# Performance work log

Measured on AMD Instinct MI355X. Metric: run time of the kernel, lower is better.

Reference implementation:

```python
import jax, jax.numpy as jnp
import numpy as np

BN_EPS = 1e-5


def setup_inputs() -> dict:
    key = jax.random.key(0)
    ks = jax.random.split(key, 9)
    B, C, H, W = 2, 64, 128, 128
    Ci = 32  # inter_channels
    sc = 0.05
    x = jax.random.normal(ks[0], (B, C, H, W), jnp.float32)
    g_w = jax.random.normal(ks[1], (Ci, C), jnp.float32) * sc
    g_b = jax.random.normal(ks[2], (Ci,), jnp.float32) * sc
    theta_w = jax.random.normal(ks[3], (Ci, C), jnp.float32) * sc
    theta_b = jax.random.normal(ks[4], (Ci,), jnp.float32) * sc
    phi_w = jax.random.normal(ks[5], (Ci, C), jnp.float32) * sc
    phi_b = jax.random.normal(ks[6], (Ci,), jnp.float32) * sc
    w_w = jax.random.normal(ks[7], (C, Ci), jnp.float32) * sc
    w_b = jnp.zeros((C,), jnp.float32)
    # BatchNorm affine params (random so the block is non-trivial; the torch
    # code zero-inits them, which would make the whole block an identity).
    bn_gamma = 1.0 + 0.1 * jax.random.normal(ks[8], (C,), jnp.float32)
    bn_beta = jnp.zeros((C,), jnp.float32)
    return dict(x=x, g_w=g_w, g_b=g_b, theta_w=theta_w, theta_b=theta_b,
                phi_w=phi_w, phi_b=phi_b, w_w=w_w, w_b=w_b,
                bn_gamma=bn_gamma, bn_beta=bn_beta)


def reference(x, g_w, g_b, theta_w, theta_b, phi_w, phi_b, w_w, w_b,
              bn_gamma, bn_beta):
    B, C, H, W = x.shape
    Ci = g_w.shape[0]
    H1, W1 = H // 2, W // 2

    def block(xq):  # embedded-gaussian non-local block on one quadrant group [B,C,h,w]
        b, c, h, w = xq.shape
        n = h * w
        xf = xq.reshape(b, c, n)                                  # [B,C,N]
        th = jnp.einsum('oc,bcn->bno', theta_w, xf) + theta_b     # [B,N,Ci]
        ph = jnp.einsum('oc,bcn->bon', phi_w, xf) + phi_b[:, None]  # [B,Ci,N]
        gx = jnp.einsum('oc,bcn->bno', g_w, xf) + g_b             # [B,N,Ci]
        f = jnp.einsum('bno,bom->bnm', th, ph)                    # [B,N,N] affinity
        a = jax.nn.softmax(f, axis=-1)
        y = jnp.einsum('bnm,bmo->bno', a, gx)                     # [B,N,Ci]
        wy = jnp.einsum('co,bno->bcn', w_w, y) + w_b[:, None]     # [B,C,N]
        wy = wy.reshape(b, c, h, w)
        # BatchNorm2d, training-mode batch stats (per quadrant call in torch)
        mu = wy.mean(axis=(0, 2, 3), keepdims=True)
        var = wy.var(axis=(0, 2, 3), keepdims=True)
        bn = (wy - mu) * jax.lax.rsqrt(var + BN_EPS)
        bn = bn * bn_gamma[None, :, None, None] + bn_beta[None, :, None, None]
        return bn + xq                                            # residual

    # split into 4 quadrants: [B,C,H,W] -> [4,B,C,H1,W1] (quadrant-major)
    xq = x.reshape(B, C, 2, H1, 2, W1).transpose(2, 4, 0, 1, 3, 5)
    xq = xq.reshape(4, B, C, H1, W1)
    zq = jax.vmap(block)(xq)                                      # [4,B,C,H1,W1]
    # reassemble
    z = zq.reshape(2, 2, B, C, H1, W1).transpose(2, 3, 0, 4, 1, 5)
    return z.reshape(B, C, H, W)
```

## Files before the change

kernel.cpp:

```cpp
#include <hip/hip_runtime.h>
#include <stdint.h>

typedef __bf16 bf16x8 __attribute__((ext_vector_type(8)));
typedef short  short4v __attribute__((ext_vector_type(4)));
typedef float  floatx4 __attribute__((ext_vector_type(4)));
typedef uint32_t u32x4 __attribute__((ext_vector_type(4)));

#define DI __device__ __forceinline__

DI uint16_t bf1(float a) {
    union { __bf16 h; uint16_t u; } r; r.h = (__bf16)a; return r.u;
}

__global__ __launch_bounds__(256) void proj_kernel(
    const float* __restrict__ x,
    const float* __restrict__ tw, const float* __restrict__ tb,
    const float* __restrict__ pw, const float* __restrict__ pb,
    const float* __restrict__ gw, const float* __restrict__ gb,
    uint16_t* __restrict__ th, uint16_t* __restrict__ phT,
    uint16_t* __restrict__ vP)
{
    __shared__ uint16_t ldsg[32 * 68];
    int nt = blockIdx.x & 63, blk = blockIdx.x >> 6;
    int tid = threadIdx.x, wid = tid >> 6, lane = tid & 63;
    int quad = lane >> 4, low = lane & 15;

    int b = blk & 1, q = blk >> 1, qh = q >> 1, qw = q & 1;
    int pixA = wid * 16 + low;
    const float* xg = x + (size_t)b * 1048576 +
                      (size_t)(qh * 64 + nt) * 128 + qw * 64 + pixA;

    float a0[8], a1[8];
#pragma unroll
    for (int j = 0; j < 8; ++j) {
        a0[j] = xg[(size_t)(quad * 8 + j) * 16384];
        a1[j] = xg[(size_t)(32 + quad * 8 + j) * 16384];
    }
    bf16x8 A0, A1;
#pragma unroll
    for (int j = 0; j < 8; ++j) {
        A0[j] = (__bf16)a0[j];
        A1[j] = (__bf16)a1[j];
    }

    auto dotile = [&](const float* W, const float* Bv, int o0) -> floatx4 {
        floatx4 acc;
        float bias = Bv[o0 + low];
#pragma unroll
        for (int r = 0; r < 4; ++r) acc[r] = bias;
        const float* wr = W + (o0 + low) * 64 + quad * 8;
        floatx4 w0a = *(const floatx4*)(wr);
        floatx4 w0b = *(const floatx4*)(wr + 4);
        floatx4 w1a = *(const floatx4*)(wr + 32);
        floatx4 w1b = *(const floatx4*)(wr + 36);
        bf16x8 B0, B1;
#pragma unroll
        for (int j = 0; j < 4; ++j) {
            B0[j]     = (__bf16)w0a[j];
            B0[j + 4] = (__bf16)w0b[j];
            B1[j]     = (__bf16)w1a[j];
            B1[j + 4] = (__bf16)w1b[j];
        }
        acc = __builtin_amdgcn_mfma_f32_16x16x32_bf16(A0, B0, acc, 0, 0, 0);
        acc = __builtin_amdgcn_mfma_f32_16x16x32_bf16(A1, B1, acc, 0, 0, 0);
        return acc;
    };

    size_t thbase = ((size_t)blk * 4096 + nt * 64 + wid * 16 + quad * 4) * 32;

    floatx4 t0 = dotile(tw, tb, 0), t1 = dotile(tw, tb, 16);
#pragma unroll
    for (int r = 0; r < 4; ++r) {
        th[thbase + r * 32 + low]      = bf1(t0[r] * 1.44269504088896f);
        th[thbase + r * 32 + 16 + low] = bf1(t1[r] * 1.44269504088896f);
    }
    floatx4 p0 = dotile(pw, pb, 0), p1 = dotile(pw, pb, 16);
#pragma unroll
    for (int r = 0; r < 4; ++r) {
        phT[thbase + r * 32 + low]      = bf1(p0[r]);
        phT[thbase + r * 32 + 16 + low] = bf1(p1[r]);
    }
    floatx4 g0 = dotile(gw, gb, 0), g1 = dotile(gw, gb, 16);
#pragma unroll
    for (int r = 0; r < 4; ++r) {
        ldsg[(low)      * 68 + wid * 16 + quad * 4 + r] = bf1(g0[r]);
        ldsg[(16 + low) * 68 + wid * 16 + quad * 4 + r] = bf1(g1[r]);
    }
    __syncthreads();
    {
        int o = tid >> 3, k = (tid & 7) * 8;
        const uint16_t* src = &ldsg[o * 68 + k];
        uint64_t lo = *(const uint64_t*)(src);
        uint64_t hi = *(const uint64_t*)(src + 4);
        union { uint64_t q[2]; u32x4 v; } out;
        out.q[0] = lo; out.q[1] = hi;
        *(u32x4*)(vP + (size_t)blk * 131072 + nt * 2048 + tid * 8) = out.v;
    }
}

__global__ __launch_bounds__(512, 2) void flash_kernel(
    const uint16_t* __restrict__ th, const uint16_t* __restrict__ phT,
    const uint16_t* __restrict__ vP, const float* __restrict__ w_w,
    const float* __restrict__ w_b, float* __restrict__ wy,
    float2* __restrict__ partials)
{
    __shared__ uint16_t ldsK[2][2][2][64 * 40];
    __shared__ uint16_t ldsV[2][2][2][32 * 72];
    __shared__ float sred[4][64][2];
    int blk = blockIdx.x & 7;
    int rg  = blockIdx.x >> 3;
    int tid = threadIdx.x, wid = tid >> 6, lane = tid & 63;
    int half = wid >> 2, w4 = wid & 3;
    int ltid = tid & 255;
    int quad = lane >> 4, low = lane & 15;
    int n0 = rg * 128 + w4 * 32;

    const uint16_t* thB = th  + (size_t)blk * 131072;
    const uint16_t* kG  = phT + (size_t)blk * 131072;
    const uint16_t* vG  = vP  + (size_t)blk * 131072;

    bf16x8 qfA = *(const bf16x8*)(thB + (n0 + low) * 32 + quad * 8);
    bf16x8 qfB = *(const bf16x8*)(thB + (n0 + 16 + low) * 32 + quad * 8);

    const int kWr = (ltid >> 2) * 40 + (ltid & 3) * 8;
    const int vWr = (ltid >> 3) * 72 + (ltid & 7) * 8;
    const u32x4* kSrc = (const u32x4*)kG + half * 8192 + ltid;
    const u32x4* vSrc = (const u32x4*)vG + half * 8192 + ltid;

    u32x4 kr0 = kSrc[0],  kr1 = kSrc[256];
    u32x4 vr0 = vSrc[0],  vr1 = vSrc[256];
    *(u32x4*)(&ldsK[half][0][0][kWr]) = kr0;  *(u32x4*)(&ldsK[half][0][1][kWr]) = kr1;
    *(u32x4*)(&ldsV[half][0][0][vWr]) = vr0;  *(u32x4*)(&ldsV[half][0][1][vWr]) = vr1;
    __syncthreads();

    floatx4 zero = {0.f, 0.f, 0.f, 0.f};
    floatx4 oaA0 = zero, oaA1 = zero, osA = zero;
    floatx4 oaB0 = zero, oaB1 = zero, osB = zero;
    union { uint32_t u[2]; short4v v; } ones;
    ones.u[0] = 0x3F803F80u; ones.u[1] = 0x3F803F80u;

    for (int t = 0; t < 16; ++t) {
        int buf = t & 1;
        if (t < 15) {
            kr0 = kSrc[(2*t + 2) * 256]; kr1 = kSrc[(2*t + 3) * 256];
            vr0 = vSrc[(2*t + 2) * 256]; vr1 = vSrc[(2*t + 3) * 256];
        }
#pragma unroll
        for (int s = 0; s < 2; ++s) {
            const uint16_t* Kb = ldsK[half][buf][s];
            const uint16_t* Vb = ldsV[half][buf][s];
            bf16x8  kf[4]; short4v va[4], vb[4];
#pragma unroll
            for (int c = 0; c < 4; ++c) {
                kf[c] = *(const bf16x8*)(Kb + (c * 16 + low) * 40 + quad * 8);
                va[c] = *(const short4v*)(Vb + low * 72 + c * 16 + quad * 4);
                vb[c] = *(const short4v*)(Vb + (16 + low) * 72 + c * 16 + quad * 4);
            }
            floatx4 saA[4], saB[4];
#pragma unroll
            for (int c = 0; c < 4; ++c) {
                saA[c] = __builtin_amdgcn_mfma_f32_16x16x32_bf16(kf[c], qfA, zero, 0, 0, 0);
                saB[c] = __builtin_amdgcn_mfma_f32_16x16x32_bf16(kf[c], qfB, zero, 0, 0, 0);
            }
            union { __bf16 h[4]; short4v v; } PA[4], PB[4];
#pragma unroll
            for (int c = 0; c < 4; ++c) {
                PA[c].h[0] = (__bf16)__builtin_amdgcn_exp2f(saA[c][0]);
                PA[c].h[1] = (__bf16)__builtin_amdgcn_exp2f(saA[c][1]);
                PA[c].h[2] = (__bf16)__builtin_amdgcn_exp2f(saA[c][2]);
                PA[c].h[3] = (__bf16)__builtin_amdgcn_exp2f(saA[c][3]);
                PB[c].h[0] = (__bf16)__builtin_amdgcn_exp2f(saB[c][0]);
                PB[c].h[1] = (__bf16)__builtin_amdgcn_exp2f(saB[c][1]);
                PB[c].h[2] = (__bf16)__builtin_amdgcn_exp2f(saB[c][2]);
                PB[c].h[3] = (__bf16)__builtin_amdgcn_exp2f(saB[c][3]);
            }
#pragma unroll
            for (int c = 0; c < 4; ++c) {
                oaA0 = __builtin_amdgcn_mfma_f32_16x16x16bf16_1k(va[c], PA[c].v, oaA0, 0, 0, 0);
                oaB0 = __builtin_amdgcn_mfma_f32_16x16x16bf16_1k(va[c], PB[c].v, oaB0, 0, 0, 0);
                oaA1 = __builtin_amdgcn_mfma_f32_16x16x16bf16_1k(vb[c], PA[c].v, oaA1, 0, 0, 0);
                oaB1 = __builtin_amdgcn_mfma_f32_16x16x16bf16_1k(vb[c], PB[c].v, oaB1, 0, 0, 0);
                osA  = __builtin_amdgcn_mfma_f32_16x16x16bf16_1k(ones.v, PA[c].v, osA, 0, 0, 0);
                osB  = __builtin_amdgcn_mfma_f32_16x16x16bf16_1k(ones.v, PB[c].v, osB, 0, 0, 0);
            }
        }
        if (t < 15) {
            *(u32x4*)(&ldsK[half][buf ^ 1][0][kWr]) = kr0;
            *(u32x4*)(&ldsK[half][buf ^ 1][1][kWr]) = kr1;
            *(u32x4*)(&ldsV[half][buf ^ 1][0][vWr]) = vr0;
            *(u32x4*)(&ldsV[half][buf ^ 1][1][vWr]) = vr1;
        }
        __syncthreads();
    }

    {
        float* exM = (float*)(&ldsK[half][0][0][0]);
        int li = ltid * 18;
#pragma unroll
        for (int r = 0; r < 4; ++r) {
            exM[li + r]      = oaA0[r];
            exM[li + 4 + r]  = oaA1[r];
            exM[li + 9 + r]  = oaB0[r];
            exM[li + 13 + r] = oaB1[r];
        }
        exM[li + 8]  = osA[0];
        exM[li + 17] = osB[0];
    }
    __syncthreads();
    const float* exO = (const float*)(&ldsK[half ^ 1][0][0][0]);
    float osA0 = osA[0] + exO[ltid * 18 + 8];
    float osB0 = osB[0] + exO[ltid * 18 + 17];
#pragma unroll
    for (int r = 0; r < 4; ++r) {
        oaA0[r] += exO[ltid * 18 + r];
        oaA1[r] += exO[ltid * 18 + 4 + r];
        oaB0[r] += exO[ltid * 18 + 9 + r];
        oaB1[r] += exO[ltid * 18 + 13 + r];
    }

    float rinvA = 1.0f / osA0, rinvB = 1.0f / osB0;
    union { __bf16 h[4]; short4v v; } YA0, YA1, YB0, YB1;
#pragma unroll
    for (int r = 0; r < 4; ++r) {
        YA0.h[r] = (__bf16)(oaA0[r] * rinvA);
        YA1.h[r] = (__bf16)(oaA1[r] * rinvA);
        YB0.h[r] = (__bf16)(oaB0[r] * rinvB);
        YB1.h[r] = (__bf16)(oaB1[r] * rinvB);
    }

    float* wyB = wy + (size_t)blk * 262144;
    int nA = n0 + low, nB = n0 + 16 + low;
#pragma unroll
    for (int cc = 0; cc < 2; ++cc) {
        int ct = half * 2 + cc;
        floatx4 accA, accB;
#pragma unroll
        for (int r = 0; r < 4; ++r) {
            accA[r] = w_b[ct * 16 + quad * 4 + r];
            accB[r] = accA[r];
        }
        floatx4 w0 = *(const floatx4*)(w_w + (ct * 16 + low) * 32 + quad * 4);
        floatx4 w1 = *(const floatx4*)(w_w + (ct * 16 + low) * 32 + 16 + quad * 4);
        union { __bf16 h[4]; short4v v; } W0, W1;
#pragma unroll
        for (int r = 0; r < 4; ++r) {
            W0.h[r] = (__bf16)w0[r];
            W1.h[r] = (__bf16)w1[r];
        }
        accA = __builtin_amdgcn_mfma_f32_16x16x16bf16_1k(W0.v, YA0.v, accA, 0, 0, 0);
        accA = __builtin_amdgcn_mfma_f32_16x16x16bf16_1k(W1.v, YA1.v, accA, 0, 0, 0);
        accB = __builtin_amdgcn_mfma_f32_16x16x16bf16_1k(W0.v, YB0.v, accB, 0, 0, 0);
        accB = __builtin_amdgcn_mfma_f32_16x16x16bf16_1k(W1.v, YB1.v, accB, 0, 0, 0);
#pragma unroll
        for (int r = 0; r < 4; ++r) {
            int ch = ct * 16 + quad * 4 + r;
            wyB[(size_t)ch * 4096 + nA] = accA[r];
            wyB[(size_t)ch * 4096 + nB] = accB[r];
            float s = accA[r] + accB[r];
            float ss = accA[r] * accA[r] + accB[r] * accB[r];
            s += __shfl_xor(s, 1); ss += __shfl_xor(ss, 1);
            s += __shfl_xor(s, 2); ss += __shfl_xor(ss, 2);
            s += __shfl_xor(s, 4); ss += __shfl_xor(ss, 4);
            s += __shfl_xor(s, 8); ss += __shfl_xor(ss, 8);
            if (low == 0) {
                sred[w4][ch][0] = s;
                sred[w4][ch][1] = ss;
            }
        }
    }
    __syncthreads();
    if (tid < 64) {
        float s  = sred[0][tid][0] + sred[1][tid][0] + sred[2][tid][0] + sred[3][tid][0];
        float ss = sred[0][tid][1] + sred[1][tid][1] + sred[2][tid][1] + sred[3][tid][1];
        partials[((size_t)blk * 32 + rg) * 64 + tid] = make_float2(s, ss);
    }
}

__global__ __launch_bounds__(64) void stats_kernel(
    const float2* __restrict__ partials, const float* __restrict__ gamma,
    const float* __restrict__ beta, float2* __restrict__ stats)
{
    int q = blockIdx.x >> 6, c = blockIdx.x & 63;
    int t = threadIdx.x;
    int b = t >> 5, rg = t & 31;
    int blk = q * 2 + b;
    float2 p = partials[((size_t)blk * 32 + rg) * 64 + c];
    float S = p.x, SS = p.y;
    S += __shfl_xor(S, 1);  SS += __shfl_xor(SS, 1);
    S += __shfl_xor(S, 2);  SS += __shfl_xor(SS, 2);
    S += __shfl_xor(S, 4);  SS += __shfl_xor(SS, 4);
    S += __shfl_xor(S, 8);  SS += __shfl_xor(SS, 8);
    S += __shfl_xor(S, 16); SS += __shfl_xor(SS, 16);
    S += __shfl_xor(S, 32); SS += __shfl_xor(SS, 32);
    if (t == 0) {
        float mu  = S * (1.0f / 8192.0f);
        float var = SS * (1.0f / 8192.0f) - mu * mu;
        float scale = gamma[c] * rsqrtf(var + 1e-5f);
        float shift = beta[c] - mu * scale;
        stats[q * 64 + c] = make_float2(scale, shift);
    }
}

__global__ __launch_bounds__(256) void final_kernel(
    const float* __restrict__ wy, const float2* __restrict__ stats,
    const float* __restrict__ x, float* __restrict__ out)
{
    size_t base = ((size_t)blockIdx.x * 256 + threadIdx.x) * 4;
    int n   = (int)(base & 4095);
    int c   = (int)((base >> 12) & 63);
    int blk = (int)(base >> 18);
    int b = blk & 1, q = blk >> 1, qh = q >> 1, qw = q & 1;
    int i = n >> 6, j = n & 63;
    float2 sc = stats[q * 64 + c];
    floatx4 wv = *(const floatx4*)(wy + base);
    size_t xa = ((size_t)(b * 64 + c) * 128 + (qh * 64 + i)) * 128 + qw * 64 + j;
    floatx4 xv = *(const floatx4*)(x + xa);
    floatx4 ov;
#pragma unroll
    for (int k = 0; k < 4; ++k) ov[k] = wv[k] * sc.x + sc.y + xv[k];
    *(floatx4*)(out + xa) = ov;
}

extern "C" void kernel_launch(void* const* d_in, const int* in_sizes, int n_in,
                              void* d_out, int out_size, void* d_ws, size_t ws_size,
                              hipStream_t stream)
{
    const float* x       = (const float*)d_in[0];
    const float* g_w     = (const float*)d_in[1];
    const float* g_b     = (const float*)d_in[2];
    const float* theta_w = (const float*)d_in[3];
    const float* theta_b = (const float*)d_in[4];
    const float* phi_w   = (const float*)d_in[5];
    const float* phi_b   = (const float*)d_in[6];
    const float* w_w     = (const float*)d_in[7];
    const float* w_b     = (const float*)d_in[8];
    const float* gamma   = (const float*)d_in[9];
    const float* beta    = (const float*)d_in[10];

    char* ws = (char*)d_ws;
    uint16_t* th       = (uint16_t*)(ws);
    uint16_t* phT      = (uint16_t*)(ws + (2u << 20));
    uint16_t* vP       = (uint16_t*)(ws + (4u << 20));
    float*    wy       = (float*)(ws + (6u << 20));
    float2*   partials = (float2*)(ws + (14u << 20));
    float2*   stats    = (float2*)(ws + (14u << 20) + (1u << 18));

    proj_kernel  <<<512,  256, 0, stream>>>(x, theta_w, theta_b, phi_w, phi_b,
                                            g_w, g_b, th, phT, vP);
    flash_kernel <<<256,  512, 0, stream>>>(th, phT, vP, w_w, w_b, wy, partials);
    stats_kernel <<<256,  64,  0, stream>>>(partials, gamma, beta, stats);
    final_kernel <<<2048, 256, 0, stream>>>(wy, stats, x, (float*)d_out);
}
```

Baseline: 128.1 us.

## Split flash kernel keys four ways over half-size query tiles, doubling grid

The flash kernel now handles 64 query rows per block instead of 128 and splits the key sequence into four spans, one per wave pair, instead of two. The grid doubles to 512 blocks and the launch bounds request four blocks per CU, which is meant to raise occupancy and latency hiding across the machine. The cross-span reduction becomes a four-way LDS sum, and each wave pair now computes only one channel tile of the output projection. The stats kernel is updated for the new partials layout. The trade-off is more redundant K/V loading per query row and tighter register limits, which could cause spills.

```diff
diff --git a/kernel.cpp b/kernel.cpp
--- a/kernel.cpp
+++ b/kernel.cpp
@@ -98,22 +98,22 @@
     }
 }
 
-__global__ __launch_bounds__(512, 2) void flash_kernel(
+__global__ __launch_bounds__(512, 4) void flash_kernel(
     const uint16_t* __restrict__ th, const uint16_t* __restrict__ phT,
     const uint16_t* __restrict__ vP, const float* __restrict__ w_w,
     const float* __restrict__ w_b, float* __restrict__ wy,
     float2* __restrict__ partials)
 {
-    __shared__ uint16_t ldsK[2][2][2][64 * 40];
-    __shared__ uint16_t ldsV[2][2][2][32 * 72];
-    __shared__ float sred[4][64][2];
+    __shared__ uint16_t ldsK[4][2][64 * 40];
+    __shared__ uint16_t ldsV[4][2][32 * 72];
+    __shared__ float sred[2][64][2];
     int blk = blockIdx.x & 7;
     int rg  = blockIdx.x >> 3;
     int tid = threadIdx.x, wid = tid >> 6, lane = tid & 63;
-    int half = wid >> 2, w4 = wid & 3;
-    int ltid = tid & 255;
+    int sp = wid >> 1, qg = wid & 1;
+    int lt = tid & 127;
     int quad = lane >> 4, low = lane & 15;
-    int n0 = rg * 128 + w4 * 32;
+    int n0 = rg * 64 + qg * 32;
 
     const uint16_t* thB = th  + (size_t)blk * 131072;
     const uint16_t* kG  = phT + (size_t)blk * 131072;
@@ -122,15 +122,17 @@
     bf16x8 qfA = *(const bf16x8*)(thB + (n0 + low) * 32 + quad * 8);
     bf16x8 qfB = *(const bf16x8*)(thB + (n0 + 16 + low) * 32 + quad * 8);
 
-    const int kWr = (ltid >> 2) * 40 + (ltid & 3) * 8;
-    const int vWr = (ltid >> 3) * 72 + (ltid & 7) * 8;
-    const u32x4* kSrc = (const u32x4*)kG + half * 8192 + ltid;
-    const u32x4* vSrc = (const u32x4*)vG + half * 8192 + ltid;
-
-    u32x4 kr0 = kSrc[0],  kr1 = kSrc[256];
-    u32x4 vr0 = vSrc[0],  vr1 = vSrc[256];
-    *(u32x4*)(&ldsK[half][0][0][kWr]) = kr0;  *(u32x4*)(&ldsK[half][0][1][kWr]) = kr1;
-    *(u32x4*)(&ldsV[half][0][0][vWr]) = vr0;  *(u32x4*)(&ldsV[half][0][1][vWr]) = vr1;
+    const u32x4* kSrc = (const u32x4*)kG + sp * 4096 + lt;
+    const u32x4* vSrc = (const u32x4*)vG + sp * 4096 + lt;
+    const int kW0 = ((lt >> 2)) * 40 + (lt & 3) * 8;
+    const int kW1 = (32 + (lt >> 2)) * 40 + (lt & 3) * 8;
+    const int vW0 = ((lt >> 3)) * 72 + (lt & 7) * 8;
+    const int vW1 = (16 + (lt >> 3)) * 72 + (lt & 7) * 8;
+
+    u32x4 kr0 = kSrc[0], kr1 = kSrc[128];
+    u32x4 vr0 = vSrc[0], vr1 = vSrc[128];
+    *(u32x4*)(&ldsK[sp][0][kW0]) = kr0;  *(u32x4*)(&ldsK[sp][0][kW1]) = kr1;
+    *(u32x4*)(&ldsV[sp][0][vW0]) = vr0;  *(u32x4*)(&ldsV[sp][0][vW1]) = vr1;
     __syncthreads();
 
     floatx4 zero = {0.f, 0.f, 0.f, 0.f};
@@ -142,97 +144,114 @@
     for (int t = 0; t < 16; ++t) {
         int buf = t & 1;
         if (t < 15) {
-            kr0 = kSrc[(2*t + 2) * 256]; kr1 = kSrc[(2*t + 3) * 256];
-            vr0 = vSrc[(2*t + 2) * 256]; vr1 = vSrc[(2*t + 3) * 256];
-        }
-#pragma unroll
-        for (int s = 0; s < 2; ++s) {
-            const uint16_t* Kb = ldsK[half][buf][s];
-            const uint16_t* Vb = ldsV[half][buf][s];
-            bf16x8  kf[4]; short4v va[4], vb[4];
+            kr0 = kSrc[(t + 1) * 256];  kr1 = kSrc[(t + 1) * 256 + 128];
+            vr0 = vSrc[(t + 1) * 256];  vr1 = vSrc[(t + 1) * 256 + 128];
+        }
+        const uint16_t* Kb = ldsK[sp][buf];
+        const uint16_t* Vb = ldsV[sp][buf];
+        bf16x8  kf[4]; short4v va[4], vb[4];
+#pragma unroll
+        for (int c = 0; c < 4; ++c) {
+            kf[c] = *(const bf16x8*)(Kb + (c * 16 + low) * 40 + quad * 8);
+            va[c] = *(const short4v*)(Vb + low * 72 + c * 16 + quad * 4);
+            vb[c] = *(const short4v*)(Vb + (16 + low) * 72 + c * 16 + quad * 4);
+        }
+        {
+            floatx4 sa[4];
+#pragma unroll
+            for (int c = 0; c < 4; ++c)
+                sa[c] = __builtin_amdgcn_mfma_f32_16x16x32_bf16(kf[c], qfA, zero, 0, 0, 0);
+            union { __bf16 h[4]; short4v v; } P[4];
 #pragma unroll
             for (int c = 0; c < 4; ++c) {
-                kf[c] = *(const bf16x8*)(Kb + (c * 16 + low) * 40 + quad * 8);
-                va[c] = *(const short4v*)(Vb + low * 72 + c * 16 + quad * 4);
-                vb[c] = *(const short4v*)(Vb + (16 + low) * 72 + c * 16 + quad * 4);
-            }
-            floatx4 saA[4], saB[4];
+                P[c].h[0] = (__bf16)__builtin_amdgcn_exp2f(sa[c][0]);
+                P[c].h[1] = (__bf16)__builtin_amdgcn_exp2f(sa[c][1]);
+                P[c].h[2] = (__bf16)__builtin_amdgcn_exp2f(sa[c][2]);
+                P[c].h[3] = (__bf16)__builtin_amdgcn_exp2f(sa[c][3]);
+            }
 #pragma unroll
             for (int c = 0; c < 4; ++c) {
-                saA[c] = __builtin_amdgcn_mfma_f32_16x16x32_bf16(kf[c], qfA, zero, 0, 0, 0);
-                saB[c] = __builtin_amdgcn_mfma_f32_16x16x32_bf16(kf[c], qfB, zero, 0, 0, 0);
-            }
-            union { __bf16 h[4]; short4v v; } PA[4], PB[4];
+                oaA0 = __builtin_amdgcn_mfma_f32_16x16x16bf16_1k(va[c], P[c].v, oaA0, 0, 0, 0);
+                oaA1 = __builtin_amdgcn_mfma_f32_16x16x16bf16_1k(vb[c], P[c].v, oaA1, 0, 0, 0);
+                osA  = __builtin_amdgcn_mfma_f32_16x16x16bf16_1k(ones.v, P[c].v, osA, 0, 0, 0);
+            }
+        }
+        {
+            floatx4 sa[4];
+#pragma unroll
+            for (int c = 0; c < 4; ++c)
+                sa[c] = __builtin_amdgcn_mfma_f32_16x16x32_bf16(kf[c], qfB, zero, 0, 0, 0);
+            union { __bf16 h[4]; short4v v; } P[4];
 #pragma unroll
             for (int c = 0; c < 4; ++c) {
-                PA[c].h[0] = (__bf16)__builtin_amdgcn_exp2f(saA[c][0]);
-                PA[c].h[1] = (__bf16)__builtin_amdgcn_exp2f(saA[c][1]);
-                PA[c].h[2] = (__bf16)__builtin_amdgcn_exp2f(saA[c][2]);
-                PA[c].h[3] = (__bf16)__builtin_amdgcn_exp2f(saA[c][3]);
-                PB[c].h[0] = (__bf16)__builtin_amdgcn_exp2f(saB[c][0]);
-                PB[c].h[1] = (__bf16)__builtin_amdgcn_exp2f(saB[c][1]);
-                PB[c].h[2] = (__bf16)__builtin_amdgcn_exp2f(saB[c][2]);
-                PB[c].h[3] = (__bf16)__builtin_amdgcn_exp2f(saB[c][3]);
+                P[c].h[0] = (__bf16)__builtin_amdgcn_exp2f(sa[c][0]);
+                P[c].h[1] = (__bf16)__builtin_amdgcn_exp2f(sa[c][1]);
+                P[c].h[2] = (__bf16)__builtin_amdgcn_exp2f(sa[c][2]);
+                P[c].h[3] = (__bf16)__builtin_amdgcn_exp2f(sa[c][3]);
             }
 #pragma unroll
             for (int c = 0; c < 4; ++c) {
-                oaA0 = __builtin_amdgcn_mfma_f32_16x16x16bf16_1k(va[c], PA[c].v, oaA0, 0, 0, 0);
-                oaB0 = __builtin_amdgcn_mfma_f32_16x16x16bf16_1k(va[c], PB[c].v, oaB0, 0, 0, 0);
-                oaA1 = __builtin_amdgcn_mfma_f32_16x16x16bf16_1k(vb[c], PA[c].v, oaA1, 0, 0, 0);
-                oaB1 = __builtin_amdgcn_mfma_f32_16x16x16bf16_1k(vb[c], PB[c].v, oaB1, 0, 0, 0);
-                osA  = __builtin_amdgcn_mfma_f32_16x16x16bf16_1k(ones.v, PA[c].v, osA, 0, 0, 0);
-                osB  = __builtin_amdgcn_mfma_f32_16x16x16bf16_1k(ones.v, PB[c].v, osB, 0, 0, 0);
+                oaB0 = __builtin_amdgcn_mfma_f32_16x16x16bf16_1k(va[c], P[c].v, oaB0, 0, 0, 0);
+                oaB1 = __builtin_amdgcn_mfma_f32_16x16x16bf16_1k(vb[c], P[c].v, oaB1, 0, 0, 0);
+                osB  = __builtin_amdgcn_mfma_f32_16x16x16bf16_1k(ones.v, P[c].v, osB, 0, 0, 0);
             }
         }
         if (t < 15) {
-            *(u32x4*)(&ldsK[half][buf ^ 1][0][kWr]) = kr0;
-            *(u32x4*)(&ldsK[half][buf ^ 1][1][kWr]) = kr1;
-            *(u32x4*)(&ldsV[half][buf ^ 1][0][vWr]) = vr0;
-            *(u32x4*)(&ldsV[half][buf ^ 1][1][vWr]) = vr1;
+            *(u32x4*)(&ldsK[sp][buf ^ 1][kW0]) = kr0;
+            *(u32x4*)(&ldsK[sp][buf ^ 1][kW1]) = kr1;
+            *(u32x4*)(&ldsV[sp][buf ^ 1][vW0]) = vr0;
+            *(u32x4*)(&ldsV[sp][buf ^ 1][vW1]) = vr1;
         }
         __syncthreads();
     }
 
     {
-        float* exM = (float*)(&ldsK[half][0][0][0]);
-        int li = ltid * 18;
+        float* exW = (float*)(&ldsK[0][0][0]);
+        int li = tid * 18;
 #pragma unroll
         for (int r = 0; r < 4; ++r) {
-            exM[li + r]      = oaA0[r];
-            exM[li + 4 + r]  = oaA1[r];
-            exM[li + 9 + r]  = oaB0[r];
-            exM[li + 13 + r] = oaB1[r];
-        }
-        exM[li + 8]  = osA[0];
-        exM[li + 17] = osB[0];
+            exW[li + r]      = oaA0[r];
+            exW[li + 4 + r]  = oaA1[r];
+            exW[li + 9 + r]  = oaB0[r];
+            exW[li + 13 + r] = oaB1[r];
+        }
+        exW[li + 8]  = osA[0];
+        exW[li + 17] = osB[0];
     }
     __syncthreads();
-    const float* exO = (const float*)(&ldsK[half ^ 1][0][0][0]);
-    float osA0 = osA[0] + exO[ltid * 18 + 8];
-    float osB0 = osB[0] + exO[ltid * 18 + 17];
+    floatx4 cA0 = zero, cA1 = zero, cB0 = zero, cB1 = zero;
+    float cosA = 0.f, cosB = 0.f;
+    {
+        const float* exR = (const float*)(&ldsK[0][0][0]);
+#pragma unroll
+        for (int s = 0; s < 4; ++s) {
+            const float* p = exR + (s * 128 + lt) * 18;
+#pragma unroll
+            for (int r = 0; r < 4; ++r) {
+                cA0[r] += p[r];
+                cA1[r] += p[4 + r];
+                cB0[r] += p[9 + r];
+                cB1[r] += p[13 + r];
+            }
+            cosA += p[8];
+            cosB += p[17];
+        }
+    }
+
+    float rinvA = 1.0f / cosA, rinvB = 1.0f / cosB;
+    union { __bf16 h[4]; short4v v; } YA0, YA1, YB0, YB1;
 #pragma unroll
     for (int r = 0; r < 4; ++r) {
-        oaA0[r] += exO[ltid * 18 + r];
-        oaA1[r] += exO[ltid * 18 + 4 + r];
-        oaB0[r] += exO[ltid * 18 + 9 + r];
-        oaB1[r] += exO[ltid * 18 + 13 + r];
-    }
-
-    float rinvA = 1.0f / osA0, rinvB = 1.0f / osB0;
-    union { __bf16 h[4]; short4v v; } YA0, YA1, YB0, YB1;
-#pragma unroll
-    for (int r = 0; r < 4; ++r) {
-        YA0.h[r] = (__bf16)(oaA0[r] * rinvA);
-        YA1.h[r] = (__bf16)(oaA1[r] * rinvA);
-        YB0.h[r] = (__bf16)(oaB0[r] * rinvB);
-        YB1.h[r] = (__bf16)(oaB1[r] * rinvB);
+        YA0.h[r] = (__bf16)(cA0[r] * rinvA);
+        YA1.h[r] = (__bf16)(cA1[r] * rinvA);
+        YB0.h[r] = (__bf16)(cB0[r] * rinvB);
+        YB1.h[r] = (__bf16)(cB1[r] * rinvB);
     }
 
     float* wyB = wy + (size_t)blk * 262144;
     int nA = n0 + low, nB = n0 + 16 + low;
-#pragma unroll
-    for (int cc = 0; cc < 2; ++cc) {
-        int ct = half * 2 + cc;
+    int ct = sp;
+    {
         floatx4 accA, accB;
 #pragma unroll
         for (int r = 0; r < 4; ++r) {
@@ -263,16 +282,16 @@
             s += __shfl_xor(s, 4); ss += __shfl_xor(ss, 4);
             s += __shfl_xor(s, 8); ss += __shfl_xor(ss, 8);
             if (low == 0) {
-                sred[w4][ch][0] = s;
-                sred[w4][ch][1] = ss;
+                sred[qg][ch][0] = s;
+                sred[qg][ch][1] = ss;
             }
         }
     }
     __syncthreads();
     if (tid < 64) {
-        float s  = sred[0][tid][0] + sred[1][tid][0] + sred[2][tid][0] + sred[3][tid][0];
-        float ss = sred[0][tid][1] + sred[1][tid][1] + sred[2][tid][1] + sred[3][tid][1];
-        partials[((size_t)blk * 32 + rg) * 64 + tid] = make_float2(s, ss);
+        float s  = sred[0][tid][0] + sred[1][tid][0];
+        float ss = sred[0][tid][1] + sred[1][tid][1];
+        partials[((size_t)blk * 64 + rg) * 64 + tid] = make_float2(s, ss);
     }
 }
 
@@ -282,10 +301,9 @@
 {
     int q = blockIdx.x >> 6, c = blockIdx.x & 63;
     int t = threadIdx.x;
-    int b = t >> 5, rg = t & 31;
-    int blk = q * 2 + b;
-    float2 p = partials[((size_t)blk * 32 + rg) * 64 + c];
-    float S = p.x, SS = p.y;
+    float2 p0 = partials[(((size_t)(q * 2 + 0)) * 64 + t) * 64 + c];
+    float2 p1 = partials[(((size_t)(q * 2 + 1)) * 64 + t) * 64 + c];
+    float S = p0.x + p1.x, SS = p0.y + p1.y;
     S += __shfl_xor(S, 1);  SS += __shfl_xor(SS, 1);
     S += __shfl_xor(S, 2);  SS += __shfl_xor(SS, 2);
     S += __shfl_xor(S, 4);  SS += __shfl_xor(SS, 4);
@@ -347,7 +365,7 @@
 
     proj_kernel  <<<512,  256, 0, stream>>>(x, theta_w, theta_b, phi_w, phi_b,
                                             g_w, g_b, th, phT, vP);
-    flash_kernel <<<256,  512, 0, stream>>>(th, phT, vP, w_w, w_b, wy, partials);
+    flash_kernel <<<512,  512, 0, stream>>>(th, phT, vP, w_w, w_b, wy, partials);
     stats_kernel <<<256,  64,  0, stream>>>(partials, gamma, beta, stats);
     final_kernel <<<2048, 256, 0, stream>>>(wy, stats, x, (float*)d_out);
 }
```

Result: faster. 123.7 us (-3.4%).
